# Performance work log

Hardware: AMD Instinct MI355X
Metric: run time of the kernel (lower is better)

Reference implementation:

```python
import jax, jax.numpy as jnp
import numpy as np

N = 100          # node_num (pinned by linear2 in_features = 1000 = N*10)
F_IN = 27        # node_feature_size
E = 262144       # number of edges
EMB = 128        # embedding_size
BN_EPS = 1e-5


def gcn_conv(x, W, b, src, dst, ew):
    """PyG GCNConv with edge weights: symmetric norm + self loops (fill=1)."""
    xw = x @ W  # [N, out]
    deg = jax.ops.segment_sum(ew, dst, num_segments=N) + 1.0  # self-loop weight 1
    dinv = jnp.where(deg > 0, deg ** -0.5, 0.0)
    norm = dinv[src] * ew * dinv[dst]              # [E]
    msg = norm[:, None] * xw[src]                  # [E, out] gather + scale
    agg = jax.ops.segment_sum(msg, dst, num_segments=N)
    agg = agg + (dinv * dinv)[:, None] * xw        # self-loop contribution
    return agg + b


def setup_inputs() -> dict:
    key = jax.random.key(0)
    ks = jax.random.split(key, 16)
    def lin(k, fan_in, shape):
        bound = 1.0 / np.sqrt(fan_in)
        return jax.random.uniform(k, shape, jnp.float32, -bound, bound)
    return {
        "x": jax.random.normal(ks[0], (1, N, F_IN), jnp.float32),
        "edge_index": jax.random.randint(ks[1], (1, 2, E), 0, N, jnp.int32),
        "edge_attr": jax.random.uniform(ks[2], (1, E), jnp.float32),
        "W1": lin(ks[3], F_IN, (F_IN, 64)),  "b1": lin(ks[4], F_IN, (64,)),
        "W2": lin(ks[5], 64, (64, 128)),     "b2": lin(ks[6], 64, (128,)),
        "W3": lin(ks[7], 128, (128, 256)),   "b3": lin(ks[8], 128, (256,)),
        "gamma": jnp.ones((256,), jnp.float32), "beta": jnp.zeros((256,), jnp.float32),
        "lw1": lin(ks[9], 256, (10, 256)),   "lb1": lin(ks[10], 256, (10,)),
        "lw2": lin(ks[11], 1000, (EMB, 1000)), "lb2": lin(ks[12], 1000, (EMB,)),
    }


def reference(x, edge_index, edge_attr, W1, b1, W2, b2, W3, b3,
              gamma, beta, lw1, lb1, lw2, lb2):
    h = x[0].reshape(N, -1)
    src, dst = edge_index[0, 0], edge_index[0, 1]
    ew = edge_attr[0]
    h = jax.nn.relu(gcn_conv(h, W1, b1, src, dst, ew))
    h = jax.nn.relu(gcn_conv(h, W2, b2, src, dst, ew))
    h = jax.nn.relu(gcn_conv(h, W3, b3, src, dst, ew))
    # BatchNorm1d (training-mode batch stats, biased var)
    mu = jnp.mean(h, axis=0)
    var = jnp.mean((h - mu) ** 2, axis=0)
    h = (h - mu) * jax.lax.rsqrt(var + BN_EPS) * gamma + beta
    # scatter_max with index=arange(N) is the identity permutation -> no-op
    h = (h @ lw1.T + lb1).reshape(-1)  # [N*10] = [1000]
    h = jax.nn.relu(h)
    return h @ lw2.T + lb2             # [EMB]
```

## Files before the change

### kernel.cpp

```cpp
#include <hip/hip_runtime.h>

#define NN 100
#define EE 262144
#define NP 64

#define WS_SSUM 640000
#define WS_MS   650000
#define WS_DI   650512
#define WS_A    650624
#define WS_H1   660624
#define WS_H2   667024
#define WS_H3   679824
#define WS_Y    705424

__global__ __launch_bounds__(512) void scatter_kernel(
    const int* __restrict__ ei, const float* __restrict__ ew,
    float* __restrict__ P)
{
    __shared__ float hist[NN * NN];
    const int tid = threadIdx.x, blk = blockIdx.x;
    for (int i = tid; i < 2500; i += 512)
        ((float4*)hist)[i] = make_float4(0.f, 0.f, 0.f, 0.f);
    __syncthreads();
    const int base = blk * 1024;
#pragma unroll
    for (int q = base + tid; q < base + 1024; q += 512) {
        int4   s4 = ((const int4*)ei)[q];
        int4   d4 = ((const int4*)(ei + EE))[q];
        float4 w4 = ((const float4*)ew)[q];
        atomicAdd(&hist[d4.x * NN + s4.x], w4.x);
        atomicAdd(&hist[d4.y * NN + s4.y], w4.y);
        atomicAdd(&hist[d4.z * NN + s4.z], w4.z);
        atomicAdd(&hist[d4.w * NN + s4.w], w4.w);
    }
    __syncthreads();
    float4* out = (float4*)(P + blk * 10000);
    for (int i = tid; i < 2500; i += 512) out[i] = ((const float4*)hist)[i];
}

__global__ __launch_bounds__(256) void rowsum_kernel(
    const float* __restrict__ P, float* __restrict__ Ssum,
    float* __restrict__ dinvg, float* __restrict__ MS)
{
    __shared__ float row[NN];
    __shared__ float part[25];
    const int tid = threadIdx.x, d = blockIdx.x;
    if (d == 0 && tid < 128)
        ((float4*)MS)[tid] = make_float4(0.f, 0.f, 0.f, 0.f);
    if (tid < NN) row[tid] = 0.f;
    __syncthreads();
    if (tid < 250) {
        int c4 = tid % 25, p0 = tid / 25;
        float4 acc = make_float4(0.f, 0.f, 0.f, 0.f);
        for (int p = p0; p < NP; p += 10) {
            float4 v = ((const float4*)P)[p * 2500 + d * 25 + c4];
            acc.x += v.x; acc.y += v.y; acc.z += v.z; acc.w += v.w;
        }
        atomicAdd(&row[c4 * 4 + 0], acc.x);
        atomicAdd(&row[c4 * 4 + 1], acc.y);
        atomicAdd(&row[c4 * 4 + 2], acc.z);
        atomicAdd(&row[c4 * 4 + 3], acc.w);
    }
    __syncthreads();
    if (tid < NN) Ssum[d * NN + tid] = row[tid];
    if (tid < 25) {
        float4 v = ((const float4*)row)[tid];
        part[tid] = v.x + v.y + v.z + v.w;
    }
    __syncthreads();
    if (tid == 0) {
        float deg = 1.f;
#pragma unroll
        for (int i = 0; i < 25; ++i) deg += part[i];
        dinvg[d] = rsqrtf(deg);
    }
}

__global__ __launch_bounds__(256) void a_l1_kernel(
    const float* __restrict__ Ssum, const float* __restrict__ dinvg,
    const float* __restrict__ x, const float* __restrict__ W1,
    const float* __restrict__ b1, float* __restrict__ Ag,
    float* __restrict__ h1g)
{
    __shared__ float xl[NN * 27];
    __shared__ float dv[NN];
    __shared__ float Arow[NN];
    __shared__ float g1[27];
    const int tid = threadIdx.x, d = blockIdx.x;
    for (int i = tid; i < NN * 27; i += 256) xl[i] = x[i];
    if (tid < NN) dv[tid] = dinvg[tid];
    __syncthreads();
    if (tid < NN) {
        float v = dv[d] * dv[tid] * Ssum[d * NN + tid];
        if (tid == d) v += dv[d] * dv[d];
        Arow[tid] = v;
        Ag[d * NN + tid] = v;
    }
    __syncthreads();
    if (tid < 27) {
        float acc = 0.f;
#pragma unroll 4
        for (int m = 0; m < NN; ++m) acc += Arow[m] * xl[m * 27 + tid];
        g1[tid] = acc;
    }
    __syncthreads();
    if (tid < 64) {
        float acc = b1[tid];
#pragma unroll
        for (int c = 0; c < 27; ++c) acc += g1[c] * W1[c * 64 + tid];
        h1g[d * 64 + tid] = fmaxf(acc, 0.f);
    }
}

__global__ __launch_bounds__(256) void l2_kernel(
    const float* __restrict__ A, const float* __restrict__ h1,
    const float* __restrict__ W2, const float* __restrict__ b2,
    float* __restrict__ h2)
{
    __shared__ float h1l[NN * 64];
    __shared__ float Ar[NN];
    __shared__ float g2[64];
    const int tid = threadIdx.x, n = blockIdx.x;
    for (int i = tid; i < NN * 16; i += 256)
        ((float4*)h1l)[i] = ((const float4*)h1)[i];
    if (tid < NN) Ar[tid] = A[n * NN + tid];
    __syncthreads();
    if (tid < 64) {
        float acc = 0.f;
#pragma unroll 4
        for (int m = 0; m < NN; ++m) acc += Ar[m] * h1l[m * 64 + tid];
        g2[tid] = acc;
    }
    __syncthreads();
    if (tid < 128) {
        float acc = b2[tid];
#pragma unroll 8
        for (int c = 0; c < 64; ++c) acc += g2[c] * W2[c * 128 + tid];
        h2[n * 128 + tid] = fmaxf(acc, 0.f);
    }
}

__global__ __launch_bounds__(256) void l3_kernel(
    const float* __restrict__ A, const float* __restrict__ h2,
    const float* __restrict__ W3, const float* __restrict__ b3,
    float* __restrict__ h3, float* __restrict__ MS)
{
    __shared__ float h2l[NN * 128];
    __shared__ float Ar[NN];
    __shared__ float g3[128];
    const int tid = threadIdx.x, n = blockIdx.x;
    for (int i = tid; i < NN * 32; i += 256)
        ((float4*)h2l)[i] = ((const float4*)h2)[i];
    if (tid < NN) Ar[tid] = A[n * NN + tid];
    __syncthreads();
    if (tid < 128) {
        float acc = 0.f;
#pragma unroll 4
        for (int m = 0; m < NN; ++m) acc += Ar[m] * h2l[m * 128 + tid];
        g3[tid] = acc;
    }
    __syncthreads();
    {
        int j = tid;
        float acc = b3[j];
#pragma unroll 8
        for (int c = 0; c < 128; ++c) acc += g3[c] * W3[c * 256 + j];
        float v = fmaxf(acc, 0.f);
        h3[n * 256 + j] = v;
        atomicAdd(&MS[j], v);
        atomicAdd(&MS[256 + j], v * v);
    }
}

__global__ __launch_bounds__(64) void lin1_kernel(
    const float* __restrict__ h3, const float* __restrict__ ms,
    const float* __restrict__ gamma, const float* __restrict__ beta,
    const float* __restrict__ lw1, const float* __restrict__ lb1,
    float* __restrict__ y)
{
    __shared__ float v[256];
    const int lane = threadIdx.x, n = blockIdx.x;
    {
        int c0 = lane * 4;
        float4 h  = *(const float4*)(h3 + n * 256 + c0);
        float4 s1 = *(const float4*)(ms + c0);
        float4 s2 = *(const float4*)(ms + 256 + c0);
        float4 gm = *(const float4*)(gamma + c0);
        float4 bt = *(const float4*)(beta + c0);
        float4 r;
#define BNAP(f) { \
        float mu = s1.f * 0.01f; \
        float var = s2.f * 0.01f - mu * mu; \
        float sc = gm.f * rsqrtf(var + 1e-5f); \
        r.f = h.f * sc + (bt.f - mu * sc); }
        BNAP(x) BNAP(y) BNAP(z) BNAP(w)
#undef BNAP
        *(float4*)(v + c0) = r;
    }
    __syncthreads();
    const int c0 = lane * 4;
    float4 hv = *(const float4*)(v + c0);
#pragma unroll
    for (int k = 0; k < 10; ++k) {
        float4 w = *(const float4*)(lw1 + k * 256 + c0);
        float acc = hv.x * w.x + hv.y * w.y + hv.z * w.z + hv.w * w.w;
#pragma unroll
        for (int off = 32; off; off >>= 1) acc += __shfl_down(acc, off);
        if (lane == 0) y[n * 10 + k] = fmaxf(acc + lb1[k], 0.f);
    }
}

__global__ __launch_bounds__(64) void lin2_kernel(
    const float* __restrict__ y, const float* __restrict__ lw2,
    const float* __restrict__ lb2, float* __restrict__ out)
{
    const int lane = threadIdx.x, j = blockIdx.x;
    const float4* y4 = (const float4*)y;
    const float4* w4 = (const float4*)(lw2 + j * 1000);
    float acc = 0.f;
#pragma unroll
    for (int i = lane; i < 250; i += 64) {
        float4 a = y4[i], b = w4[i];
        acc += a.x * b.x + a.y * b.y + a.z * b.z + a.w * b.w;
    }
#pragma unroll
    for (int off = 32; off; off >>= 1) acc += __shfl_down(acc, off);
    if (lane == 0) out[j] = acc + lb2[j];
}

extern "C" void kernel_launch(void* const* d_in, const int* in_sizes, int n_in,
                              void* d_out, int out_size, void* d_ws, size_t ws_size,
                              hipStream_t stream) {
    const float* x     = (const float*)d_in[0];
    const int*   ei    = (const int*)d_in[1];
    const float* ew    = (const float*)d_in[2];
    const float* W1    = (const float*)d_in[3];
    const float* b1    = (const float*)d_in[4];
    const float* W2    = (const float*)d_in[5];
    const float* b2    = (const float*)d_in[6];
    const float* W3    = (const float*)d_in[7];
    const float* b3    = (const float*)d_in[8];
    const float* gamma = (const float*)d_in[9];
    const float* beta  = (const float*)d_in[10];
    const float* lw1   = (const float*)d_in[11];
    const float* lb1   = (const float*)d_in[12];
    const float* lw2   = (const float*)d_in[13];
    const float* lb2   = (const float*)d_in[14];

    float* ws   = (float*)d_ws;
    float* P    = ws;
    float* Ssum = ws + WS_SSUM;
    float* MS   = ws + WS_MS;
    float* dinv = ws + WS_DI;
    float* A    = ws + WS_A;
    float* h1   = ws + WS_H1;
    float* h2   = ws + WS_H2;
    float* h3   = ws + WS_H3;
    float* y    = ws + WS_Y;
    float* out  = (float*)d_out;

    scatter_kernel<<<NP, 512, 0, stream>>>(ei, ew, P);
    rowsum_kernel<<<NN, 256, 0, stream>>>(P, Ssum, dinv, MS);
    a_l1_kernel<<<NN, 256, 0, stream>>>(Ssum, dinv, x, W1, b1, A, h1);
    l2_kernel<<<NN, 256, 0, stream>>>(A, h1, W2, b2, h2);
    l3_kernel<<<NN, 256, 0, stream>>>(A, h2, W3, b3, h3, MS);
    lin1_kernel<<<NN, 64, 0, stream>>>(h3, MS, gamma, beta, lw1, lb1, y);
    lin2_kernel<<<128, 64, 0, stream>>>(y, lw2, lb2, out);
}
```

Before: 130.4 us.

## Fold rowsum into scatter/a_l1 and fuse lin1+lin2 into one tail kernel

Removes the rowsum kernel. Scatter blocks now write per-block degree partials, and a_l1 reduces the partial histograms and degrees directly. lin1 and lin2 are merged into one tail kernel: each of the 128 blocks recomputes the full BN+lin1 output (1000 values), with the BN scale folded into the lw1 weights, before its lin2 dot product. This cuts two launches and their inter-kernel gaps, at the cost of redundant lin1 work in every block and more reads of P in a_l1.

```diff
diff --git a/kernel.cpp b/kernel.cpp
--- a/kernel.cpp
+++ b/kernel.cpp
@@ -4,23 +4,24 @@
 #define EE 262144
 #define NP 64
 
-#define WS_SSUM 640000
-#define WS_MS   650000
-#define WS_DI   650512
-#define WS_A    650624
-#define WS_H1   660624
-#define WS_H2   667024
-#define WS_H3   679824
-#define WS_Y    705424
+#define WS_D   640000
+#define WS_MS  646400
+#define WS_A   646912
+#define WS_H1  656912
+#define WS_H2  663312
+#define WS_H3  676112
 
 __global__ __launch_bounds__(512) void scatter_kernel(
     const int* __restrict__ ei, const float* __restrict__ ew,
-    float* __restrict__ P)
+    float* __restrict__ P, float* __restrict__ D, float* __restrict__ MS)
 {
     __shared__ float hist[NN * NN];
+    __shared__ float part[NN][4];
     const int tid = threadIdx.x, blk = blockIdx.x;
     for (int i = tid; i < 2500; i += 512)
         ((float4*)hist)[i] = make_float4(0.f, 0.f, 0.f, 0.f);
+    if (blk == 0 && tid < 128)
+        ((float4*)MS)[tid] = make_float4(0.f, 0.f, 0.f, 0.f);
     __syncthreads();
     const int base = blk * 1024;
 #pragma unroll
@@ -34,50 +35,23 @@
         atomicAdd(&hist[d4.w * NN + s4.w], w4.w);
     }
     __syncthreads();
-    float4* out = (float4*)(P + blk * 10000);
-    for (int i = tid; i < 2500; i += 512) out[i] = ((const float4*)hist)[i];
-}
-
-__global__ __launch_bounds__(256) void rowsum_kernel(
-    const float* __restrict__ P, float* __restrict__ Ssum,
-    float* __restrict__ dinvg, float* __restrict__ MS)
-{
-    __shared__ float row[NN];
-    __shared__ float part[25];
-    const int tid = threadIdx.x, d = blockIdx.x;
-    if (d == 0 && tid < 128)
-        ((float4*)MS)[tid] = make_float4(0.f, 0.f, 0.f, 0.f);
-    if (tid < NN) row[tid] = 0.f;
-    __syncthreads();
-    if (tid < 250) {
-        int c4 = tid % 25, p0 = tid / 25;
-        float4 acc = make_float4(0.f, 0.f, 0.f, 0.f);
-        for (int p = p0; p < NP; p += 10) {
-            float4 v = ((const float4*)P)[p * 2500 + d * 25 + c4];
-            acc.x += v.x; acc.y += v.y; acc.z += v.z; acc.w += v.w;
-        }
-        atomicAdd(&row[c4 * 4 + 0], acc.x);
-        atomicAdd(&row[c4 * 4 + 1], acc.y);
-        atomicAdd(&row[c4 * 4 + 2], acc.z);
-        atomicAdd(&row[c4 * 4 + 3], acc.w);
-    }
-    __syncthreads();
-    if (tid < NN) Ssum[d * NN + tid] = row[tid];
-    if (tid < 25) {
-        float4 v = ((const float4*)row)[tid];
-        part[tid] = v.x + v.y + v.z + v.w;
-    }
-    __syncthreads();
-    if (tid == 0) {
-        float deg = 1.f;
-#pragma unroll
-        for (int i = 0; i < 25; ++i) deg += part[i];
-        dinvg[d] = rsqrtf(deg);
-    }
+    for (int i = tid; i < 2500; i += 512)
+        ((float4*)(P + blk * 10000))[i] = ((const float4*)hist)[i];
+    if (tid < 400) {
+        int row = tid >> 2, q = tid & 3;
+        const float* r = hist + row * NN + q * 25;
+        float s = 0.f;
+#pragma unroll
+        for (int k = 0; k < 25; ++k) s += r[k];
+        part[row][q] = s;
+    }
+    __syncthreads();
+    if (tid < NN)
+        D[blk * NN + tid] = part[tid][0] + part[tid][1] + part[tid][2] + part[tid][3];
 }
 
 __global__ __launch_bounds__(256) void a_l1_kernel(
-    const float* __restrict__ Ssum, const float* __restrict__ dinvg,
+    const float* __restrict__ P, const float* __restrict__ D,
     const float* __restrict__ x, const float* __restrict__ W1,
     const float* __restrict__ b1, float* __restrict__ Ag,
     float* __restrict__ h1g)
@@ -87,11 +61,20 @@
     __shared__ float Arow[NN];
     __shared__ float g1[27];
     const int tid = threadIdx.x, d = blockIdx.x;
+
     for (int i = tid; i < NN * 27; i += 256) xl[i] = x[i];
-    if (tid < NN) dv[tid] = dinvg[tid];
-    __syncthreads();
     if (tid < NN) {
-        float v = dv[d] * dv[tid] * Ssum[d * NN + tid];
+        float deg = 1.f;
+#pragma unroll 8
+        for (int p = 0; p < NP; ++p) deg += D[p * NN + tid];
+        dv[tid] = rsqrtf(deg);
+    }
+    __syncthreads();
+    if (tid < NN) {
+        float s = 0.f;
+#pragma unroll 8
+        for (int p = 0; p < NP; ++p) s += P[p * 10000 + d * NN + tid];
+        float v = dv[d] * dv[tid] * s;
         if (tid == d) v += dv[d] * dv[d];
         Arow[tid] = v;
         Ag[d * NN + tid] = v;
@@ -172,60 +155,71 @@
     }
 }
 
-__global__ __launch_bounds__(64) void lin1_kernel(
-    const float* __restrict__ h3, const float* __restrict__ ms,
+__global__ __launch_bounds__(256) void tail_kernel(
+    const float* __restrict__ h3g, const float* __restrict__ MS,
     const float* __restrict__ gamma, const float* __restrict__ beta,
     const float* __restrict__ lw1, const float* __restrict__ lb1,
-    float* __restrict__ y)
-{
-    __shared__ float v[256];
-    const int lane = threadIdx.x, n = blockIdx.x;
+    const float* __restrict__ lw2, const float* __restrict__ lb2,
+    float* __restrict__ out)
+{
+    __shared__ float sc[256], sh[256];
+    __shared__ float wsc[2560];
+    __shared__ float cst[10];
+    __shared__ float yl[1000];
+    __shared__ float partw[4];
+    const int tid = threadIdx.x, j = blockIdx.x;
+
     {
-        int c0 = lane * 4;
-        float4 h  = *(const float4*)(h3 + n * 256 + c0);
-        float4 s1 = *(const float4*)(ms + c0);
-        float4 s2 = *(const float4*)(ms + 256 + c0);
-        float4 gm = *(const float4*)(gamma + c0);
-        float4 bt = *(const float4*)(beta + c0);
-        float4 r;
-#define BNAP(f) { \
-        float mu = s1.f * 0.01f; \
-        float var = s2.f * 0.01f - mu * mu; \
-        float sc = gm.f * rsqrtf(var + 1e-5f); \
-        r.f = h.f * sc + (bt.f - mu * sc); }
-        BNAP(x) BNAP(y) BNAP(z) BNAP(w)
-#undef BNAP
-        *(float4*)(v + c0) = r;
-    }
-    __syncthreads();
-    const int c0 = lane * 4;
-    float4 hv = *(const float4*)(v + c0);
-#pragma unroll
-    for (int k = 0; k < 10; ++k) {
-        float4 w = *(const float4*)(lw1 + k * 256 + c0);
-        float acc = hv.x * w.x + hv.y * w.y + hv.z * w.z + hv.w * w.w;
-#pragma unroll
-        for (int off = 32; off; off >>= 1) acc += __shfl_down(acc, off);
-        if (lane == 0) y[n * 10 + k] = fmaxf(acc + lb1[k], 0.f);
-    }
-}
-
-__global__ __launch_bounds__(64) void lin2_kernel(
-    const float* __restrict__ y, const float* __restrict__ lw2,
-    const float* __restrict__ lb2, float* __restrict__ out)
-{
-    const int lane = threadIdx.x, j = blockIdx.x;
-    const float4* y4 = (const float4*)y;
-    const float4* w4 = (const float4*)(lw2 + j * 1000);
+        float s1 = MS[tid], s2 = MS[256 + tid];
+        float mu  = s1 * 0.01f;
+        float var = s2 * 0.01f - mu * mu;
+        float s   = gamma[tid] * rsqrtf(var + 1e-5f);
+        sc[tid] = s;
+        sh[tid] = beta[tid] - mu * s;
+    }
+    __syncthreads();
+    for (int i = tid; i < 2560; i += 256) wsc[i] = sc[i & 255] * lw1[i];
+    if (tid < 10) {
+        float a = lb1[tid];
+        const float* w = lw1 + tid * 256;
+#pragma unroll 4
+        for (int c = 0; c < 256; ++c) a += sh[c] * w[c];
+        cst[tid] = a;
+    }
+    __syncthreads();
+
+    if (tid < 250) {
+        int n0 = (tid / 5) * 2, k0 = (tid % 5) * 2;
+        float a00 = 0.f, a01 = 0.f, a10 = 0.f, a11 = 0.f;
+        for (int c = 0; c < 256; c += 4) {
+            float4 hA = *(const float4*)(h3g + n0 * 256 + c);
+            float4 hB = *(const float4*)(h3g + (n0 + 1) * 256 + c);
+            float4 wA = *(const float4*)(wsc + k0 * 256 + c);
+            float4 wB = *(const float4*)(wsc + (k0 + 1) * 256 + c);
+            a00 += hA.x*wA.x + hA.y*wA.y + hA.z*wA.z + hA.w*wA.w;
+            a01 += hA.x*wB.x + hA.y*wB.y + hA.z*wB.z + hA.w*wB.w;
+            a10 += hB.x*wA.x + hB.y*wA.y + hB.z*wA.z + hB.w*wA.w;
+            a11 += hB.x*wB.x + hB.y*wB.y + hB.z*wB.z + hB.w*wB.w;
+        }
+        yl[n0 * 10 + k0]           = fmaxf(a00 + cst[k0], 0.f);
+        yl[n0 * 10 + k0 + 1]       = fmaxf(a01 + cst[k0 + 1], 0.f);
+        yl[(n0 + 1) * 10 + k0]     = fmaxf(a10 + cst[k0], 0.f);
+        yl[(n0 + 1) * 10 + k0 + 1] = fmaxf(a11 + cst[k0 + 1], 0.f);
+    }
+    __syncthreads();
+
     float acc = 0.f;
-#pragma unroll
-    for (int i = lane; i < 250; i += 64) {
-        float4 a = y4[i], b = w4[i];
-        acc += a.x * b.x + a.y * b.y + a.z * b.z + a.w * b.w;
+    if (tid < 250) {
+        float4 a = ((const float4*)yl)[tid];
+        float4 b = ((const float4*)(lw2 + j * 1000))[tid];
+        acc = a.x * b.x + a.y * b.y + a.z * b.z + a.w * b.w;
     }
 #pragma unroll
     for (int off = 32; off; off >>= 1) acc += __shfl_down(acc, off);
-    if (lane == 0) out[j] = acc + lb2[j];
+    if ((tid & 63) == 0) partw[tid >> 6] = acc;
+    __syncthreads();
+    if (tid == 0)
+        out[j] = partw[0] + partw[1] + partw[2] + partw[3] + lb2[j];
 }
 
 extern "C" void kernel_launch(void* const* d_in, const int* in_sizes, int n_in,
@@ -247,23 +241,20 @@
     const float* lw2   = (const float*)d_in[13];
     const float* lb2   = (const float*)d_in[14];
 
-    float* ws   = (float*)d_ws;
-    float* P    = ws;
-    float* Ssum = ws + WS_SSUM;
-    float* MS   = ws + WS_MS;
-    float* dinv = ws + WS_DI;
-    float* A    = ws + WS_A;
-    float* h1   = ws + WS_H1;
-    float* h2   = ws + WS_H2;
-    float* h3   = ws + WS_H3;
-    float* y    = ws + WS_Y;
-    float* out  = (float*)d_out;
-
-    scatter_kernel<<<NP, 512, 0, stream>>>(ei, ew, P);
-    rowsum_kernel<<<NN, 256, 0, stream>>>(P, Ssum, dinv, MS);
-    a_l1_kernel<<<NN, 256, 0, stream>>>(Ssum, dinv, x, W1, b1, A, h1);
+    float* ws  = (float*)d_ws;
+    float* P   = ws;
+    float* D   = ws + WS_D;
+    float* MS  = ws + WS_MS;
+    float* A   = ws + WS_A;
+    float* h1  = ws + WS_H1;
+    float* h2  = ws + WS_H2;
+    float* h3  = ws + WS_H3;
+    float* out = (float*)d_out;
+
+    scatter_kernel<<<NP, 512, 0, stream>>>(ei, ew, P, D, MS);
+    a_l1_kernel<<<NN, 256, 0, stream>>>(P, D, x, W1, b1, A, h1);
     l2_kernel<<<NN, 256, 0, stream>>>(A, h1, W2, b2, h2);
     l3_kernel<<<NN, 256, 0, stream>>>(A, h2, W3, b3, h3, MS);
-    lin1_kernel<<<NN, 64, 0, stream>>>(h3, MS, gamma, beta, lw1, lb1, y);
-    lin2_kernel<<<128, 64, 0, stream>>>(y, lw2, lb2, out);
-}
+    tail_kernel<<<128, 256, 0, stream>>>(h3, MS, gamma, beta, lw1, lb1,
+                                         lw2, lb2, out);
+}
```

New measurement: 138.7 us. +6.4%, slower.
